# Performance work log

Measured on AMD Instinct MI355X. Metric: run time of the kernel, lower is better.

Reference implementation:

```python
import jax, jax.numpy as jnp
import numpy as np

N_NODES = 8192

def setup_inputs() -> dict:
    key = jax.random.key(0)
    k1, k2, k3 = jax.random.split(key, 3)
    x = jax.random.normal(k1, (N_NODES, 256), dtype=jnp.float32)
    edge_index = jax.random.randint(k2, (2, 262144), 0, N_NODES, dtype=jnp.int64)
    W = jax.random.normal(k3, (256, 128), dtype=jnp.float32) / np.sqrt(256.0)
    b = jnp.zeros((128,), dtype=jnp.float32)
    return {"x": x, "edge_index": edge_index, "W": W, "b": b}

def reference(x, edge_index, W, b):
    # PyG GCNConv: h = X W; add self-loops; sym-normalize D^-1/2 (A+I) D^-1/2; aggregate; + bias
    N = x.shape[0]
    h = x @ W  # [N, H]
    loops = jnp.arange(N, dtype=edge_index.dtype)
    src = jnp.concatenate([edge_index[0], loops])  # [E+N]
    dst = jnp.concatenate([edge_index[1], loops])
    deg = jax.ops.segment_sum(jnp.ones_like(dst, dtype=h.dtype), dst, num_segments=N)  # in-degree incl. self-loop
    dinv = jax.lax.rsqrt(deg)  # deg >= 1 due to self-loops
    norm = dinv[src] * dinv[dst]  # [E+N]
    msgs = h[src] * norm[:, None]  # gather + scale
    agg = jax.ops.segment_sum(msgs, dst, num_segments=N)  # scatter-add to targets
    z = jax.nn.relu(agg + b)  # [N, H]
    adj_recon = jax.nn.sigmoid(z @ z.T)  # [N, N]
    return adj_recon, z
```

## Files before the change

### kernel.cpp

```cpp
#include <hip/hip_runtime.h>
#include <hip/hip_bf16.h>

#define N_NODES 8192
#define E_EDGES 262144
#define HID 128
#define FIN 256
#define CAP 128

typedef __attribute__((ext_vector_type(8))) short bf16x8;
typedef __attribute__((ext_vector_type(4))) float f32x4;

__global__ __launch_bounds__(256) void xw_kernel(const float* __restrict__ x,
                                                 const float* __restrict__ W,
                                                 float* __restrict__ h,
                                                 unsigned* __restrict__ cursor) {
    if (blockIdx.x < 32) cursor[blockIdx.x * 256 + threadIdx.x] = 0u;

    int col = threadIdx.x & 127;
    int row0 = blockIdx.x * 16 + (threadIdx.x >> 7) * 8;
    const float* xr = x + (size_t)row0 * FIN;
    float acc[8];
#pragma unroll
    for (int r = 0; r < 8; ++r) acc[r] = 0.f;

    for (int k = 0; k < FIN; k += 4) {
        float4 xv[8];
#pragma unroll
        for (int r = 0; r < 8; ++r) xv[r] = *(const float4*)(xr + r * FIN + k);
#pragma unroll
        for (int kk = 0; kk < 4; ++kk) {
            float w = W[(size_t)(k + kk) * HID + col];
#pragma unroll
            for (int r = 0; r < 8; ++r)
                acc[r] = fmaf(((const float*)&xv[r])[kk], w, acc[r]);
        }
    }
#pragma unroll
    for (int r = 0; r < 8; ++r)
        h[(size_t)(row0 + r) * HID + col] = acc[r];
}

__global__ void scatter_csr(const int* __restrict__ src, const int* __restrict__ dst,
                            unsigned* __restrict__ cursor, int* __restrict__ csr_src) {
    int e = blockIdx.x * 256 + threadIdx.x;
    if (e < E_EDGES) {
        int d = dst[e];
        unsigned pos = atomicAdd(&cursor[d], 1u);
        csr_src[(size_t)d * CAP + pos] = src[e];
    }
}

__global__ __launch_bounds__(256) void agg_kernel(const float* __restrict__ h,
                                                  const unsigned* __restrict__ cnt,
                                                  const int* __restrict__ csr_src,
                                                  const float* __restrict__ b,
                                                  float* __restrict__ z_out,
                                                  __hip_bfloat16* __restrict__ zb) {
    int row = blockIdx.x;
    int slot = threadIdx.x >> 6;
    int fp = threadIdx.x & 63;
    const float2* h2 = (const float2*)h;
    const int* bin = csr_src + (size_t)row * CAP;

    float ax = 0.f, ay = 0.f;
    unsigned ne = cnt[row];
    for (unsigned e = (unsigned)slot; e < ne; e += 4) {
        int s = bin[e];
        float ds = rsqrtf((float)(cnt[s] + 1u));
        float2 hv = h2[(size_t)s * 64 + fp];
        ax = fmaf(hv.x, ds, ax);
        ay = fmaf(hv.y, ds, ay);
    }
    __shared__ float part[4][64][2];
    part[slot][fp][0] = ax;
    part[slot][fp][1] = ay;
    __syncthreads();
    if (slot == 0) {
        float di = rsqrtf((float)(ne + 1u));
        float2 hv = h2[(size_t)row * 64 + fp];
        float sx = (part[0][fp][0] + part[1][fp][0]) + (part[2][fp][0] + part[3][fp][0]) + hv.x * di;
        float sy = (part[0][fp][1] + part[1][fp][1]) + (part[2][fp][1] + part[3][fp][1]) + hv.y * di;
        float2 bb = ((const float2*)b)[fp];
        float zx = fmaxf(fmaf(sx, di, bb.x), 0.f);
        float zy = fmaxf(fmaf(sy, di, bb.y), 0.f);
        ((float2*)z_out)[(size_t)row * 64 + fp] = make_float2(zx, zy);
        unsigned short bx = __builtin_bit_cast(unsigned short, __float2bfloat16(zx));
        unsigned short by = __builtin_bit_cast(unsigned short, __float2bfloat16(zy));
        ((unsigned*)zb)[(size_t)row * 64 + fp] = ((unsigned)by << 16) | (unsigned)bx;
    }
}

__global__ __launch_bounds__(256) void gemm_sig(const __hip_bfloat16* __restrict__ zb,
                                                float* __restrict__ adj) {
    int ti = blockIdx.y;
    int tj = blockIdx.x;
    if (tj < ti) return;

    int wid = threadIdx.x >> 6;
    int lane = threadIdx.x & 63;
    int wm = wid >> 1, wn = wid & 1;
    int row0 = ti * 128 + wm * 64;
    int col0 = tj * 128 + wn * 64;
    int lr = lane & 15;
    int lk = (lane >> 4) * 8;

    f32x4 acc[4][4];
#pragma unroll
    for (int m = 0; m < 4; ++m)
#pragma unroll
        for (int n = 0; n < 4; ++n) acc[m][n] = (f32x4){0.f, 0.f, 0.f, 0.f};

#pragma unroll
    for (int ks = 0; ks < 4; ++ks) {
        int k = ks * 32 + lk;
        bf16x8 a[4], bfr[4];
#pragma unroll
        for (int m = 0; m < 4; ++m)
            a[m] = *(const bf16x8*)(zb + (size_t)(row0 + m * 16 + lr) * HID + k);
#pragma unroll
        for (int n = 0; n < 4; ++n)
            bfr[n] = *(const bf16x8*)(zb + (size_t)(col0 + n * 16 + lr) * HID + k);
#pragma unroll
        for (int m = 0; m < 4; ++m)
#pragma unroll
            for (int n = 0; n < 4; ++n)
                acc[m][n] = __builtin_amdgcn_mfma_f32_16x16x32_bf16(a[m], bfr[n], acc[m][n], 0, 0, 0);
    }

    int orow = (lane >> 4) * 4;
    bool mirror = (ti != tj);
#pragma unroll
    for (int m = 0; m < 4; ++m) {
        int rowb = row0 + m * 16 + orow;
#pragma unroll
        for (int n = 0; n < 4; ++n) {
            int col = col0 + n * 16 + lr;
            f32x4 s4;
#pragma unroll
            for (int r = 0; r < 4; ++r) {
                float v = acc[m][n][r];
                s4[r] = __builtin_amdgcn_rcpf(1.0f + __expf(-v));
            }
            *(f32x4*)(adj + (size_t)col * N_NODES + rowb) = s4;
            if (mirror) {
#pragma unroll
                for (int r = 0; r < 4; ++r)
                    adj[(size_t)(rowb + r) * N_NODES + col] = s4[r];
            }
        }
    }
}

extern "C" void kernel_launch(void* const* d_in, const int* in_sizes, int n_in,
                              void* d_out, int out_size, void* d_ws, size_t ws_size,
                              hipStream_t stream) {
    const float* x = (const float*)d_in[0];
    const int* ei = (const int*)d_in[1];
    const float* W = (const float*)d_in[2];
    const float* b = (const float*)d_in[3];
    const int* src = ei;
    const int* dst = ei + E_EDGES;

    float* adj = (float*)d_out;
    float* z_out = (float*)d_out + (size_t)N_NODES * N_NODES;

    char* ws = (char*)d_ws;
    float* h = (float*)ws;
    __hip_bfloat16* zb = (__hip_bfloat16*)(ws + (4u << 20));
    unsigned* cursor = (unsigned*)(ws + (6u << 20));
    int* csr = (int*)(ws + (6u << 20) + (32u << 10));

    hipLaunchKernelGGL(xw_kernel, dim3(N_NODES / 16), dim3(256), 0, stream, x, W, h, cursor);
    hipLaunchKernelGGL(scatter_csr, dim3(E_EDGES / 256), dim3(256), 0, stream, src, dst, cursor, csr);
    hipLaunchKernelGGL(agg_kernel, dim3(N_NODES), dim3(256), 0, stream, h, cursor, csr, b, z_out, zb);
    hipLaunchKernelGGL(gemm_sig, dim3(64, 64), dim3(256), 0, stream, zb, adj);
}
```

Before: 151.1 us.

## Fuse XW, CSR build and aggregation into one persistent kernel with grid barrier

```diff
diff --git a/kernel.cpp b/kernel.cpp
--- a/kernel.cpp
+++ b/kernel.cpp
@@ -6,87 +6,101 @@
 #define HID 128
 #define FIN 256
 #define CAP 128
+#define GRID_P 1024
 
 typedef __attribute__((ext_vector_type(8))) short bf16x8;
 typedef __attribute__((ext_vector_type(4))) float f32x4;
 
-__global__ __launch_bounds__(256) void xw_kernel(const float* __restrict__ x,
-                                                 const float* __restrict__ W,
-                                                 float* __restrict__ h,
-                                                 unsigned* __restrict__ cursor) {
-    if (blockIdx.x < 32) cursor[blockIdx.x * 256 + threadIdx.x] = 0u;
-
-    int col = threadIdx.x & 127;
-    int row0 = blockIdx.x * 16 + (threadIdx.x >> 7) * 8;
-    const float* xr = x + (size_t)row0 * FIN;
-    float acc[8];
-#pragma unroll
-    for (int r = 0; r < 8; ++r) acc[r] = 0.f;
-
-    for (int k = 0; k < FIN; k += 4) {
-        float4 xv[8];
-#pragma unroll
-        for (int r = 0; r < 8; ++r) xv[r] = *(const float4*)(xr + r * FIN + k);
-#pragma unroll
-        for (int kk = 0; kk < 4; ++kk) {
-            float w = W[(size_t)(k + kk) * HID + col];
-#pragma unroll
-            for (int r = 0; r < 8; ++r)
-                acc[r] = fmaf(((const float*)&xv[r])[kk], w, acc[r]);
-        }
+__device__ inline void gridbar(unsigned* bar, unsigned target) {
+    __syncthreads();
+    if (threadIdx.x == 0) {
+        __threadfence();
+        atomicAdd(bar, 1u);
+        while (__hip_atomic_load(bar, __ATOMIC_RELAXED, __HIP_MEMORY_SCOPE_AGENT) < target)
+            __builtin_amdgcn_s_sleep(8);
+        __threadfence();
     }
-#pragma unroll
-    for (int r = 0; r < 8; ++r)
-        h[(size_t)(row0 + r) * HID + col] = acc[r];
+    __syncthreads();
 }
 
-__global__ void scatter_csr(const int* __restrict__ src, const int* __restrict__ dst,
-                            unsigned* __restrict__ cursor, int* __restrict__ csr_src) {
-    int e = blockIdx.x * 256 + threadIdx.x;
-    if (e < E_EDGES) {
+__global__ __launch_bounds__(256, 4) void prep_fused(
+    const float* __restrict__ x, const float* __restrict__ W,
+    const int* __restrict__ src, const int* __restrict__ dst,
+    unsigned* __restrict__ cursor, int* __restrict__ csr_src,
+    const float* __restrict__ b, float* __restrict__ z_out,
+    __hip_bfloat16* __restrict__ zb, float* __restrict__ h,
+    unsigned* __restrict__ bar) {
+    int bid = blockIdx.x;
+    int tid = threadIdx.x;
+
+    {
+        int e = bid * 256 + tid;
         int d = dst[e];
         unsigned pos = atomicAdd(&cursor[d], 1u);
         csr_src[(size_t)d * CAP + pos] = src[e];
     }
-}
 
-__global__ __launch_bounds__(256) void agg_kernel(const float* __restrict__ h,
-                                                  const unsigned* __restrict__ cnt,
-                                                  const int* __restrict__ csr_src,
-                                                  const float* __restrict__ b,
-                                                  float* __restrict__ z_out,
-                                                  __hip_bfloat16* __restrict__ zb) {
-    int row = blockIdx.x;
-    int slot = threadIdx.x >> 6;
-    int fp = threadIdx.x & 63;
+    if (bid < 512) {
+        int col = tid & 127;
+        int row0 = bid * 16 + (tid >> 7) * 8;
+        const float* xr = x + (size_t)row0 * FIN;
+        float acc[8];
+#pragma unroll
+        for (int r = 0; r < 8; ++r) acc[r] = 0.f;
+        for (int k = 0; k < FIN; k += 4) {
+            float4 xv[8];
+#pragma unroll
+            for (int r = 0; r < 8; ++r) xv[r] = *(const float4*)(xr + r * FIN + k);
+#pragma unroll
+            for (int kk = 0; kk < 4; ++kk) {
+                float w = W[(size_t)(k + kk) * HID + col];
+#pragma unroll
+                for (int r = 0; r < 8; ++r)
+                    acc[r] = fmaf(((const float*)&xv[r])[kk], w, acc[r]);
+            }
+        }
+#pragma unroll
+        for (int r = 0; r < 8; ++r)
+            h[(size_t)(row0 + r) * HID + col] = acc[r];
+    }
+
+    gridbar(bar, GRID_P);
+
+    int slot = tid >> 6;
+    int fp = tid & 63;
     const float2* h2 = (const float2*)h;
-    const int* bin = csr_src + (size_t)row * CAP;
+    __shared__ float part[4][64][2];
 
-    float ax = 0.f, ay = 0.f;
-    unsigned ne = cnt[row];
-    for (unsigned e = (unsigned)slot; e < ne; e += 4) {
-        int s = bin[e];
-        float ds = rsqrtf((float)(cnt[s] + 1u));
-        float2 hv = h2[(size_t)s * 64 + fp];
-        ax = fmaf(hv.x, ds, ax);
-        ay = fmaf(hv.y, ds, ay);
-    }
-    __shared__ float part[4][64][2];
-    part[slot][fp][0] = ax;
-    part[slot][fp][1] = ay;
-    __syncthreads();
-    if (slot == 0) {
-        float di = rsqrtf((float)(ne + 1u));
-        float2 hv = h2[(size_t)row * 64 + fp];
-        float sx = (part[0][fp][0] + part[1][fp][0]) + (part[2][fp][0] + part[3][fp][0]) + hv.x * di;
-        float sy = (part[0][fp][1] + part[1][fp][1]) + (part[2][fp][1] + part[3][fp][1]) + hv.y * di;
-        float2 bb = ((const float2*)b)[fp];
-        float zx = fmaxf(fmaf(sx, di, bb.x), 0.f);
-        float zy = fmaxf(fmaf(sy, di, bb.y), 0.f);
-        ((float2*)z_out)[(size_t)row * 64 + fp] = make_float2(zx, zy);
-        unsigned short bx = __builtin_bit_cast(unsigned short, __float2bfloat16(zx));
-        unsigned short by = __builtin_bit_cast(unsigned short, __float2bfloat16(zy));
-        ((unsigned*)zb)[(size_t)row * 64 + fp] = ((unsigned)by << 16) | (unsigned)bx;
+    for (int i = 0; i < 8; ++i) {
+        int row = bid * 8 + i;
+        const int* bin = csr_src + (size_t)row * CAP;
+
+        float ax = 0.f, ay = 0.f;
+        unsigned ne = cursor[row];
+        for (unsigned e = (unsigned)slot; e < ne; e += 4) {
+            int s = bin[e];
+            float ds = rsqrtf((float)(cursor[s] + 1u));
+            float2 hv = h2[(size_t)s * 64 + fp];
+            ax = fmaf(hv.x, ds, ax);
+            ay = fmaf(hv.y, ds, ay);
+        }
+        part[slot][fp][0] = ax;
+        part[slot][fp][1] = ay;
+        __syncthreads();
+        if (slot == 0) {
+            float di = rsqrtf((float)(ne + 1u));
+            float2 hv = h2[(size_t)row * 64 + fp];
+            float sx = (part[0][fp][0] + part[1][fp][0]) + (part[2][fp][0] + part[3][fp][0]) + hv.x * di;
+            float sy = (part[0][fp][1] + part[1][fp][1]) + (part[2][fp][1] + part[3][fp][1]) + hv.y * di;
+            float2 bb = ((const float2*)b)[fp];
+            float zx = fmaxf(fmaf(sx, di, bb.x), 0.f);
+            float zy = fmaxf(fmaf(sy, di, bb.y), 0.f);
+            ((float2*)z_out)[(size_t)row * 64 + fp] = make_float2(zx, zy);
+            unsigned short bx = __builtin_bit_cast(unsigned short, __float2bfloat16(zx));
+            unsigned short by = __builtin_bit_cast(unsigned short, __float2bfloat16(zy));
+            ((unsigned*)zb)[(size_t)row * 64 + fp] = ((unsigned)by << 16) | (unsigned)bx;
+        }
+        __syncthreads();
     }
 }
 
@@ -168,10 +182,11 @@
     float* h = (float*)ws;
     __hip_bfloat16* zb = (__hip_bfloat16*)(ws + (4u << 20));
     unsigned* cursor = (unsigned*)(ws + (6u << 20));
-    int* csr = (int*)(ws + (6u << 20) + (32u << 10));
+    unsigned* bar = (unsigned*)(ws + (6u << 20) + (32u << 10));
+    int* csr = (int*)(ws + (6u << 20) + (64u << 10));
 
-    hipLaunchKernelGGL(xw_kernel, dim3(N_NODES / 16), dim3(256), 0, stream, x, W, h, cursor);
-    hipLaunchKernelGGL(scatter_csr, dim3(E_EDGES / 256), dim3(256), 0, stream, src, dst, cursor, csr);
-    hipLaunchKernelGGL(agg_kernel, dim3(N_NODES), dim3(256), 0, stream, h, cursor, csr, b, z_out, zb);
+    hipMemsetAsync(cursor, 0, (32u << 10) + 256, stream);
+    hipLaunchKernelGGL(prep_fused, dim3(GRID_P), dim3(256), 0, stream,
+                       x, W, src, dst, cursor, csr, b, z_out, zb, h, bar);
     hipLaunchKernelGGL(gemm_sig, dim3(64, 64), dim3(256), 0, stream, zb, adj);
 }
```

New measurement: 292.6 us. +93.6%, slower.
